# Kernel optimization log

Hardware: AMD Instinct MI355X
Metric: run time of the kernel (lower is better)

Reference implementation:

```python
import jax, jax.numpy as jnp
import numpy as np

J_NUM = 24
# SMPL kinematic tree: parents[i] < i for all i >= 1 (root has parent -1)
PARENTS = np.array([-1, 0, 0, 0, 1, 2, 3, 4, 5, 6, 7, 8, 9, 9, 9, 12, 13, 14,
                    16, 17, 18, 19, 20, 21], dtype=np.int32)
BATCH = 131072


def setup_inputs() -> dict:
    key = jax.random.key(0)
    k1, k2, k3 = jax.random.split(key, 3)
    pose = jax.random.normal(k1, (BATCH, J_NUM, 3), dtype=jnp.float32) * 0.3
    trans = jax.random.normal(k2, (BATCH, 3), dtype=jnp.float32)
    # Rest-pose joint transforms: identity rotation + random local offset (learned buffer)
    offs = jax.random.normal(k3, (J_NUM, 3), dtype=jnp.float32) * 0.1
    J = jnp.tile(jnp.eye(4, dtype=jnp.float32)[None], (J_NUM, 1, 1))
    J = J.at[:, :3, 3].set(offs)
    parents = jnp.asarray(PARENTS, dtype=jnp.int32)
    return {"pose": pose, "trans": trans, "J": J, "parents": parents}


def rodrigues(r):
    """Axis-angle [..., 3] -> rotation matrices [..., 3, 3] (batched Rodrigues)."""
    theta = jnp.sqrt(jnp.sum(r * r, axis=-1, keepdims=True) + 1e-16)  # [...,1]
    rh = r / theta
    x, y, z = rh[..., 0], rh[..., 1], rh[..., 2]
    zero = jnp.zeros_like(x)
    K = jnp.stack([zero, -z, y, z, zero, -x, -y, x, zero], axis=-1)
    K = K.reshape(r.shape[:-1] + (3, 3))
    c = jnp.cos(theta)[..., None]
    s = jnp.sin(theta)[..., None]
    outer = rh[..., :, None] * rh[..., None, :]
    I3 = jnp.eye(3, dtype=r.dtype)
    return c * I3 + (1.0 - c) * outer + s * K


def reference(pose, trans, J, parents):
    par = np.asarray(parents)  # static tree structure
    B, Jn = pose.shape[0], pose.shape[1]
    R = rodrigues(pose)                                   # [B,J,3,3]
    # embed into 4x4 homogeneous transforms
    R4 = jnp.pad(R, ((0, 0), (0, 0), (0, 1), (0, 1)))
    R4 = R4.at[:, :, 3, 3].set(1.0)                       # [B,J,4,4]
    # local transform per joint: J[i] @ localRot[i] (batched once)
    local = jnp.einsum('jab,njbc->njac', J, R4)           # [B,J,4,4]
    # sequential kinematic-tree composition (fixed small unrolled loop)
    results = [local[:, 0]]
    for i in range(1, Jn):
        results.append(jnp.matmul(results[int(par[i])], local[:, i]))
    stacked = jnp.stack(results, axis=1)                  # [B,J,4,4]
    J_posed = stacked[:, :, :3, 3] + trans[:, None, :]    # [B,J,3]
    return J_posed
```

## Files before the change

### kernel.cpp

```cpp
#include <hip/hip_runtime.h>

#define J_NUM 24


__global__ __launch_bounds__(256)
void fk_kernel(const float* __restrict__ pose, const float* __restrict__ trans,
               const float* __restrict__ Jm, float* __restrict__ out, int B)
{
    int b = blockIdx.x * blockDim.x + threadIdx.x;
    if (b >= B) return;

    const int par[J_NUM] = {-1,0,0,0,1,2,3,4,5,6,7,8,9,9,9,12,13,14,16,17,18,19,20,21};

    float p[72];
    const float4* pp = reinterpret_cast<const float4*>(pose + (size_t)b * 72);
#pragma unroll
    for (int i = 0; i < 18; ++i) {
        float4 v = pp[i];
        p[4*i+0] = v.x; p[4*i+1] = v.y; p[4*i+2] = v.z; p[4*i+3] = v.w;
    }

    float t0 = trans[(size_t)b*3 + 0];
    float t1 = trans[(size_t)b*3 + 1];
    float t2 = trans[(size_t)b*3 + 2];

    float Rc[J_NUM][9];
    float Pc[J_NUM][3];

    float* o = out + (size_t)b * (J_NUM * 3);

#pragma unroll
    for (int j = 0; j < J_NUM; ++j) {
        float rx = p[j*3+0], ry = p[j*3+1], rz = p[j*3+2];
        float tt = rx*rx + ry*ry + rz*rz + 1e-16f;
        float theta = sqrtf(tt);
        float inv = 1.0f / theta;
        float x = rx*inv, y = ry*inv, z = rz*inv;
        float c = cosf(theta), s = sinf(theta);
        float C = 1.0f - c;

        float R0 = c + C*x*x;
        float R1 = C*x*y - s*z;
        float R2 = C*x*z + s*y;
        float R3 = C*y*x + s*z;
        float R4 = c + C*y*y;
        float R5 = C*y*z - s*x;
        float R6 = C*z*x - s*y;
        float R7 = C*z*y + s*x;
        float R8 = c + C*z*z;

        float ox = Jm[j*16 + 3];
        float oy = Jm[j*16 + 7];
        float oz = Jm[j*16 + 11];

        if (j == 0) {
            Rc[0][0]=R0; Rc[0][1]=R1; Rc[0][2]=R2;
            Rc[0][3]=R3; Rc[0][4]=R4; Rc[0][5]=R5;
            Rc[0][6]=R6; Rc[0][7]=R7; Rc[0][8]=R8;
            Pc[0][0]=ox; Pc[0][1]=oy; Pc[0][2]=oz;
        } else {
            const int q = par[j];
            Pc[j][0] = Pc[q][0] + Rc[q][0]*ox + Rc[q][1]*oy + Rc[q][2]*oz;
            Pc[j][1] = Pc[q][1] + Rc[q][3]*ox + Rc[q][4]*oy + Rc[q][5]*oz;
            Pc[j][2] = Pc[q][2] + Rc[q][6]*ox + Rc[q][7]*oy + Rc[q][8]*oz;
            Rc[j][0] = Rc[q][0]*R0 + Rc[q][1]*R3 + Rc[q][2]*R6;
            Rc[j][1] = Rc[q][0]*R1 + Rc[q][1]*R4 + Rc[q][2]*R7;
            Rc[j][2] = Rc[q][0]*R2 + Rc[q][1]*R5 + Rc[q][2]*R8;
            Rc[j][3] = Rc[q][3]*R0 + Rc[q][4]*R3 + Rc[q][5]*R6;
            Rc[j][4] = Rc[q][3]*R1 + Rc[q][4]*R4 + Rc[q][5]*R7;
            Rc[j][5] = Rc[q][3]*R2 + Rc[q][4]*R5 + Rc[q][5]*R8;
            Rc[j][6] = Rc[q][6]*R0 + Rc[q][7]*R3 + Rc[q][8]*R6;
            Rc[j][7] = Rc[q][6]*R1 + Rc[q][7]*R4 + Rc[q][8]*R7;
            Rc[j][8] = Rc[q][6]*R2 + Rc[q][7]*R5 + Rc[q][8]*R8;
        }

        o[j*3+0] = Pc[j][0] + t0;
        o[j*3+1] = Pc[j][1] + t1;
        o[j*3+2] = Pc[j][2] + t2;
    }
}

extern "C" void kernel_launch(void* const* d_in, const int* in_sizes, int n_in,
                              void* d_out, int out_size, void* d_ws, size_t ws_size,
                              hipStream_t stream) {
    const float* pose  = (const float*)d_in[0];
    const float* trans = (const float*)d_in[1];
    const float* Jm    = (const float*)d_in[2];
    float* out = (float*)d_out;

    int B = in_sizes[0] / (J_NUM * 3);
    int threads = 256;
    int blocks = (B + threads - 1) / threads;
    fk_kernel<<<blocks, threads, 0, stream>>>(pose, trans, Jm, out, B);
}
```

Measured before the change: 110.8 us.

## Stage pose loads and output stores through LDS for coalesced access

Each block of 64 threads now loads its pose slice cooperatively into shared memory with coalesced float4 reads, computes FK reading poses from LDS, writes results back to LDS and then stores them with coalesced float4 writes. The previous code had each thread read and write a strided 288-byte record, which gives uncoalesced global traffic. It also switches to fast __sinf/__cosf intrinsics and a smaller block size. The bounds check is gone, so it assumes B is a multiple of 64, and the fast trig lowers precision slightly.

```diff
diff --git a/kernel.cpp b/kernel.cpp
--- a/kernel.cpp
+++ b/kernel.cpp
@@ -1,33 +1,40 @@
 #include <hip/hip_runtime.h>
 
 #define J_NUM 24
+#define BLOCK 64
+#define PER_ELEM 72
+#define LDS_FLOATS (BLOCK * PER_ELEM)
 
+__global__ __launch_bounds__(BLOCK)
+void fk_kernel(const float* __restrict__ pose, const float* __restrict__ trans,
+               const float* __restrict__ Jm, float* __restrict__ out)
+{
+    __shared__ float s[LDS_FLOATS];
 
-__global__ __launch_bounds__(256)
-void fk_kernel(const float* __restrict__ pose, const float* __restrict__ trans,
-               const float* __restrict__ Jm, float* __restrict__ out, int B)
-{
-    int b = blockIdx.x * blockDim.x + threadIdx.x;
-    if (b >= B) return;
+    const int t = threadIdx.x;
+    const size_t blockBase = (size_t)blockIdx.x * BLOCK;
+    const int b = (int)blockBase + t;
+
+    {
+        const float4* src = reinterpret_cast<const float4*>(pose + blockBase * PER_ELEM);
+        float4* dst = reinterpret_cast<float4*>(s);
+#pragma unroll
+        for (int i = 0; i < 18; ++i)
+            dst[i * BLOCK + t] = src[i * BLOCK + t];
+    }
+    __syncthreads();
+
+    const float* p = s + t * PER_ELEM;
+
+    const float t0 = trans[(size_t)b * 3 + 0];
+    const float t1 = trans[(size_t)b * 3 + 1];
+    const float t2 = trans[(size_t)b * 3 + 2];
 
     const int par[J_NUM] = {-1,0,0,0,1,2,3,4,5,6,7,8,9,9,9,12,13,14,16,17,18,19,20,21};
 
-    float p[72];
-    const float4* pp = reinterpret_cast<const float4*>(pose + (size_t)b * 72);
-#pragma unroll
-    for (int i = 0; i < 18; ++i) {
-        float4 v = pp[i];
-        p[4*i+0] = v.x; p[4*i+1] = v.y; p[4*i+2] = v.z; p[4*i+3] = v.w;
-    }
-
-    float t0 = trans[(size_t)b*3 + 0];
-    float t1 = trans[(size_t)b*3 + 1];
-    float t2 = trans[(size_t)b*3 + 2];
-
     float Rc[J_NUM][9];
     float Pc[J_NUM][3];
-
-    float* o = out + (size_t)b * (J_NUM * 3);
+    float o[PER_ELEM];
 
 #pragma unroll
     for (int j = 0; j < J_NUM; ++j) {
@@ -36,17 +43,17 @@
         float theta = sqrtf(tt);
         float inv = 1.0f / theta;
         float x = rx*inv, y = ry*inv, z = rz*inv;
-        float c = cosf(theta), s = sinf(theta);
+        float c = __cosf(theta), sn = __sinf(theta);
         float C = 1.0f - c;
 
         float R0 = c + C*x*x;
-        float R1 = C*x*y - s*z;
-        float R2 = C*x*z + s*y;
-        float R3 = C*y*x + s*z;
+        float R1 = C*x*y - sn*z;
+        float R2 = C*x*z + sn*y;
+        float R3 = C*y*x + sn*z;
         float R4 = c + C*y*y;
-        float R5 = C*y*z - s*x;
-        float R6 = C*z*x - s*y;
-        float R7 = C*z*y + s*x;
+        float R5 = C*y*z - sn*x;
+        float R6 = C*z*x - sn*y;
+        float R7 = C*z*y + sn*x;
         float R8 = c + C*z*z;
 
         float ox = Jm[j*16 + 3];
@@ -78,6 +85,20 @@
         o[j*3+1] = Pc[j][1] + t1;
         o[j*3+2] = Pc[j][2] + t2;
     }
+
+    float* mine = s + t * PER_ELEM;
+#pragma unroll
+    for (int k = 0; k < PER_ELEM; ++k) mine[k] = o[k];
+
+    __syncthreads();
+
+    {
+        const float4* src = reinterpret_cast<const float4*>(s);
+        float4* dst = reinterpret_cast<float4*>(out + blockBase * PER_ELEM);
+#pragma unroll
+        for (int i = 0; i < 18; ++i)
+            dst[i * BLOCK + t] = src[i * BLOCK + t];
+    }
 }
 
 extern "C" void kernel_launch(void* const* d_in, const int* in_sizes, int n_in,
@@ -89,7 +110,6 @@
     float* out = (float*)d_out;
 
     int B = in_sizes[0] / (J_NUM * 3);
-    int threads = 256;
-    int blocks = (B + threads - 1) / threads;
-    fk_kernel<<<blocks, threads, 0, stream>>>(pose, trans, Jm, out, B);
+    int blocks = B / BLOCK;
+    fk_kernel<<<blocks, BLOCK, 0, stream>>>(pose, trans, Jm, out);
 }
```

Measured after the change: 94.69 us. -14.5%, faster.
